# Optimization experiments

Measured on AMD Instinct MI355X. Metric: run time of the kernel, lower is better.

The kernel has to match this reference:

```python
import jax, jax.numpy as jnp
import numpy as np


def log_g(x):
    # log of g(x) = where(x>=0, x+0.5, sigmoid(x))
    return jnp.where(x >= 0, jnp.log(jax.nn.relu(x) + 0.5), -jax.nn.softplus(-x))


def heinsen_associative_scan_log(log_coeffs, log_values):
    a_star = jnp.cumsum(log_coeffs, axis=1)
    log_h0_plus_b_star = jax.lax.cumlogsumexp(log_values - a_star, axis=1)
    return jnp.exp(a_star + log_h0_plus_b_star)


def setup_inputs() -> dict:
    key = jax.random.key(0)
    k1, k2 = jax.random.split(key)
    B, T, D = 4, 8192, 512
    x = jax.random.normal(k1, (B, T, D), dtype=jnp.float32)
    # Linear(dim, 2*dim, bias=False); scaled like torch default init
    W = jax.random.normal(k2, (D, 2 * D), dtype=jnp.float32) * (1.0 / np.sqrt(D))
    return {"x": x, "W": W}


def reference(x, W):
    hg = jnp.einsum('btd,de->bte', x, W)  # [B,T,2D]
    hidden, gate = jnp.split(hg, 2, axis=-1)
    log_z = -jax.nn.softplus(-gate)       # log sigmoid(gate)
    log_coeffs = -jax.nn.softplus(gate)   # log (1 - sigmoid(gate))
    log_tilde_h = log_g(hidden)
    out = heinsen_associative_scan_log(log_coeffs, log_z + log_tilde_h)
    return out
```

## Files before the change

### kernel.cpp

```cpp
#include <hip/hip_runtime.h>

typedef unsigned short u16;
typedef unsigned int   u32;

typedef __bf16 bf16x8 __attribute__((ext_vector_type(8)));
typedef float  f32x4  __attribute__((ext_vector_type(4)));

#define B_DIM 4
#define T_DIM 8192
#define D_DIM 512
#define M_DIM (B_DIM * T_DIM)
#define K_DIM D_DIM
#define NC    256
#define LCH   32

__device__ __forceinline__ u16 f2bf(float f) {
  u32 u = __float_as_uint(f);
  u32 r = (u + 0x7FFFu + ((u >> 16) & 1u)) >> 16;
  return (u16)r;
}
__device__ __forceinline__ float bf2f(u16 b) {
  return __uint_as_float(((u32)b) << 16);
}

__device__ __forceinline__ void gload_lds16(const u16* g, u16* lds) {
  __builtin_amdgcn_global_load_lds(
      (const __attribute__((address_space(1))) void*)g,
      (__attribute__((address_space(3))) void*)lds, 16, 0, 0);
}


__global__ __launch_bounds__(256) void convert_xw(const float4* __restrict__ x4,
                                                  u16* __restrict__ xb,
                                                  const float* __restrict__ W,
                                                  u16* __restrict__ wt, int n4) {
  const int bid = blockIdx.x;
  if (bid < 2048) {
    int i = bid * 256 + threadIdx.x;
    const int stride = 2048 * 256;
    for (; i < n4; i += stride) {
      float4 f = x4[i];
      u32 w0 = (u32)f2bf(f.x) | ((u32)f2bf(f.y) << 16);
      u32 w1 = (u32)f2bf(f.z) | ((u32)f2bf(f.w) << 16);
      *reinterpret_cast<uint2*>(xb + (size_t)i * 4) = make_uint2(w0, w1);
    }
  } else {
    int idx = (bid - 2048) * 256 + threadIdx.x;
    int n  = idx & 1023;
    int k0 = (idx >> 10) * 8;
    float f[8];
#pragma unroll
    for (int j = 0; j < 8; ++j) f[j] = W[(size_t)(k0 + j) * 1024 + n];
    u32 w[4];
#pragma unroll
    for (int j = 0; j < 4; ++j)
      w[j] = (u32)f2bf(f[2 * j]) | ((u32)f2bf(f[2 * j + 1]) << 16);
    *reinterpret_cast<uint4*>(wt + (size_t)n * 512 + k0) = make_uint4(w[0], w[1], w[2], w[3]);
  }
}


#define BK 32
#define NT 16

__global__ __launch_bounds__(512, 4) void gemm_act(const u16* __restrict__ xb,
                                                   const u16* __restrict__ wt,
                                                   u32* __restrict__ av_buf,
                                                   float* __restrict__ Asum,
                                                   float* __restrict__ Bsum) {
  __shared__ u16 As[3][8192];
  __shared__ u16 Bs[3][4096];

  const int tid  = threadIdx.x;
  const int lane = tid & 63;
  const int wave = tid >> 6;
  const int l15  = lane & 15;
  const int lh   = lane >> 4;
  const int wr   = wave >> 1;
  const int wc   = wave & 1;
  const int m_base = blockIdx.x * 256;
  const int d0     = blockIdx.y * 64;

  const int pairl = tid >> 3;
  const int slog  = (tid & 7) ^ (pairl & 7);
  const int lrow  = (pairl << 1) | (slog >> 2);
  const int scol  = (slog & 3) << 3;
  const int garow0 = m_base + lrow;
  const int garow1 = garow0 + 128;
  const int pB = lrow >> 5;
  const int gn = ((pB & 1) ? 512 : 0) + d0 + ((pB >> 1) << 5) + (lrow & 31);
  const int ldsw = wave * 512;

  f32x4 acc[4][4];
#pragma unroll
  for (int m = 0; m < 4; ++m)
#pragma unroll
    for (int n = 0; n < 4; ++n)
      acc[m][n] = (f32x4){0.f, 0.f, 0.f, 0.f};

#define STAGE(buf, kt)                                                      \
  do {                                                                      \
    const int ko = (kt) * BK + scol;                                        \
    gload_lds16(xb + (size_t)garow0 * K_DIM + ko, &As[buf][ldsw]);          \
    gload_lds16(xb + (size_t)garow1 * K_DIM + ko, &As[buf][4096 + ldsw]);   \
    gload_lds16(wt + (size_t)gn * K_DIM + ko, &Bs[buf][ldsw]);              \
  } while (0)

#define AOFF(row) (((row) >> 1) * 64 + (((((((row) & 1) << 2) | lh)) ^ (((row) >> 1) & 7)) << 3))

#define COMPUTE(cur)                                                        \
  do {                                                                      \
    bf16x8 af[4], bfr[4];                                                   \
    _Pragma("unroll")                                                       \
    for (int m = 0; m < 4; ++m)                                             \
      af[m] = *reinterpret_cast<const bf16x8*>(&As[cur][AOFF(64 * wr + 16 * m + l15)]); \
    _Pragma("unroll")                                                       \
    for (int n = 0; n < 4; ++n)                                             \
      bfr[n] = *reinterpret_cast<const bf16x8*>(&Bs[cur][AOFF(64 * wc + 16 * n + l15)]); \
    _Pragma("unroll")                                                       \
    for (int m = 0; m < 4; ++m)                                             \
      _Pragma("unroll")                                                     \
      for (int n = 0; n < 4; ++n)                                           \
        acc[m][n] = __builtin_amdgcn_mfma_f32_16x16x32_bf16(af[m], bfr[n], acc[m][n], 0, 0, 0); \
  } while (0)

#define WAITV(N) asm volatile("s_waitcnt vmcnt(" #N ")" ::: "memory")
#define BAR()    asm volatile("s_barrier" ::: "memory")

  STAGE(0, 0);
  STAGE(1, 1);
#pragma unroll
  for (int t = 0; t < 14; ++t) {
    WAITV(3);
    BAR();
    STAGE((t + 2) % 3, t + 2);
    COMPUTE(t % 3);
  }
  WAITV(3); BAR(); COMPUTE(2);
  WAITV(0); BAR(); COMPUTE(0);
#undef STAGE
#undef COMPUTE
#undef WAITV
#undef BAR

  const int row_w = m_base + 64 * wr;
#pragma unroll
  for (int h = 0; h < 2; ++h) {
    float Ar[2][2], Br[2][2];
#pragma unroll
    for (int mm = 0; mm < 2; ++mm) {
      const int m = 2 * h + mm;
#pragma unroll
      for (int n = 0; n < 2; ++n) {
        float A = 1.f, Bv = 0.f;
        const int dch = d0 + 32 * wc + 16 * n + l15;
#pragma unroll
        for (int r = 0; r < 4; ++r) {
          float hid = acc[m][n][r];
          float gt  = acc[m][n + 2][r];
          float e   = __expf(gt);
          float inv = 1.f / (1.f + e);
          float g   = (hid >= 0.f) ? (hid + 0.5f) : (1.f / (1.f + __expf(-hid)));
          float v   = (e * inv) * g;
          u16 abf = f2bf(inv);
          u16 vbf = f2bf(v);
          const int grow = row_w + 16 * m + 4 * lh + r;
          av_buf[(size_t)grow * D_DIM + dch] = (u32)abf | ((u32)vbf << 16);
          float afv = bf2f(abf), vfv = bf2f(vbf);
          Bv = afv * Bv + vfv;
          A *= afv;
        }
        Ar[n][mm] = A; Br[n][mm] = Bv;
      }
    }
#pragma unroll
    for (int n = 0; n < 2; ++n)
#pragma unroll
      for (int mm = 0; mm < 2; ++mm) {
        float A = Ar[n][mm], Bv = Br[n][mm];
#pragma unroll
        for (int d = 1; d <= 2; d <<= 1) {
          float pA = __shfl(A, lane - 16 * d);
          float pB = __shfl(Bv, lane - 16 * d);
          if (lh >= d) { Bv = A * pB + Bv; A = A * pA; }
        }
        Ar[n][mm] = A; Br[n][mm] = Bv;
      }
    if (lh == 3) {
      const int grow = row_w + 32 * h;
      const int b = grow >> 13;
      const int c = (grow & 8191) >> 5;
      const size_t o = ((size_t)(b * NC + c)) * D_DIM;
#pragma unroll
      for (int n = 0; n < 2; ++n) {
        const int dch = d0 + 32 * wc + 16 * n + l15;
        float Ac = Ar[n][0] * Ar[n][1];
        float Bc = Ar[n][1] * Br[n][0] + Br[n][1];
        Asum[o + dch] = Ac;
        Bsum[o + dch] = Bc;
      }
    }
  }
}


__global__ __launch_bounds__(256) void scan_pass2(const float* __restrict__ Asum,
                                                  const float* __restrict__ Bsum,
                                                  float* __restrict__ carry) {
  const int w    = (blockIdx.x << 2) + (threadIdx.x >> 6);
  const int lane = threadIdx.x & 63;
  const int b = w >> 9;
  const int d = w & 511;
  const size_t base = ((size_t)(b * NC + lane * 4)) * D_DIM + d;
  float A[4], Bv[4];
#pragma unroll
  for (int i = 0; i < 4; ++i) {
    A[i]  = Asum[base + (size_t)i * D_DIM];
    Bv[i] = Bsum[base + (size_t)i * D_DIM];
  }
  float La = 1.f, Lb = 0.f;
#pragma unroll
  for (int i = 0; i < 4; ++i) { Lb = A[i] * Lb + Bv[i]; La *= A[i]; }
  float Sa = La, Sb = Lb;
#pragma unroll
  for (int dlt = 1; dlt < 64; dlt <<= 1) {
    float pa = __shfl_up(Sa, dlt, 64);
    float pb = __shfl_up(Sb, dlt, 64);
    if (lane >= dlt) { Sb = Sa * pb + Sb; Sa = Sa * pa; }
  }
  float Eb = __shfl_up(Sb, 1, 64);
  float h = (lane == 0) ? 0.f : Eb;
#pragma unroll
  for (int i = 0; i < 4; ++i) {
    carry[base + (size_t)i * D_DIM] = h;
    h = A[i] * h + Bv[i];
  }
}


__global__ __launch_bounds__(256) void scan_pass3(const u32* __restrict__ av_buf,
                                                  const float2* __restrict__ carry,
                                                  float2* __restrict__ out) {
  const int c  = blockIdx.x;
  const int b  = blockIdx.y;
  const int d2 = threadIdx.x;
  float2 hh = carry[((size_t)(b * NC + c)) * 256 + d2];
  float h0 = hh.x, h1 = hh.y;
  const size_t rowbase = (size_t)b * T_DIM + (size_t)c * LCH;
  for (int t = 0; t < LCH; ++t) {
    const size_t idx = (rowbase + t) * 256 + d2;
    uint2 w = reinterpret_cast<const uint2*>(av_buf)[idx];
    h0 = bf2f(w.x & 0xffff) * h0 + bf2f(w.x >> 16);
    h1 = bf2f(w.y & 0xffff) * h1 + bf2f(w.y >> 16);
    out[idx] = make_float2(h0, h1);
  }
}


extern "C" void kernel_launch(void* const* d_in, const int* in_sizes, int n_in,
                              void* d_out, int out_size, void* d_ws, size_t ws_size,
                              hipStream_t stream) {
  const float* x = (const float*)d_in[0];
  const float* W = (const float*)d_in[1];
  float* out = (float*)d_out;

  char* ws = (char*)d_ws;
  u16*   xb     = (u16*)(ws + 0);
  u16*   wtp    = (u16*)(ws + 33554432);
  u32*   av_buf = (u32*)(ws + 34603008);
  float* Asum   = (float*)(ws + 101711872);
  float* Bsum   = (float*)(ws + 103809024);
  float* carry  = (float*)(ws + 105906176);
  if (ws_size < 108003328ULL) return;

  convert_xw<<<2304, 256, 0, stream>>>((const float4*)x, xb, W, wtp, (M_DIM * K_DIM) / 4);
  gemm_act<<<dim3(M_DIM / 256, D_DIM / 64), 512, 0, stream>>>(xb, wtp, av_buf, Asum, Bsum);
  scan_pass2<<<512, 256, 0, stream>>>(Asum, Bsum, carry);
  scan_pass3<<<dim3(NC, B_DIM), 256, 0, stream>>>(av_buf, (const float2*)carry, (float2*)out);
}
```

Measured before the change: 109.5 us.

## Double K-tile to 64 and interleave loads with prioritized MFMA clusters

After: 122.0 us. 11.4% more time.

```diff
diff --git a/kernel.cpp b/kernel.cpp
--- a/kernel.cpp
+++ b/kernel.cpp
@@ -60,16 +60,16 @@
 }
 
 
-#define BK 32
-#define NT 16
-
-__global__ __launch_bounds__(512, 4) void gemm_act(const u16* __restrict__ xb,
+#define BK 64
+#define NTL 8
+
+__global__ __launch_bounds__(512, 2) void gemm_act(const u16* __restrict__ xb,
                                                    const u16* __restrict__ wt,
                                                    u32* __restrict__ av_buf,
                                                    float* __restrict__ Asum,
                                                    float* __restrict__ Bsum) {
-  __shared__ u16 As[3][8192];
-  __shared__ u16 Bs[3][4096];
+  __shared__ u16 As[3][16384];
+  __shared__ u16 Bs[3][8192];
 
   const int tid  = threadIdx.x;
   const int lane = tid & 63;
@@ -81,15 +81,16 @@
   const int m_base = blockIdx.x * 256;
   const int d0     = blockIdx.y * 64;
 
-  const int pairl = tid >> 3;
-  const int slog  = (tid & 7) ^ (pairl & 7);
-  const int lrow  = (pairl << 1) | (slog >> 2);
-  const int scol  = (slog & 3) << 3;
-  const int garow0 = m_base + lrow;
-  const int garow1 = garow0 + 128;
-  const int pB = lrow >> 5;
-  const int gn = ((pB & 1) ? 512 : 0) + d0 + ((pB >> 1) << 5) + (lrow & 31);
+  const int arow = tid >> 3;
+  const int acol = (((tid & 7) ^ (arow & 7)) << 3);
   const int ldsw = wave * 512;
+  int gnc[2];
+#pragma unroll
+  for (int c = 0; c < 2; ++c) {
+    int j = c * 64 + arow;
+    int p = j >> 5;
+    gnc[c] = ((p & 1) ? 512 : 0) + d0 + ((p >> 1) << 5) + (j & 31);
+  }
 
   f32x4 acc[4][4];
 #pragma unroll
@@ -98,49 +99,90 @@
     for (int n = 0; n < 4; ++n)
       acc[m][n] = (f32x4){0.f, 0.f, 0.f, 0.f};
 
-#define STAGE(buf, kt)                                                      \
+#define SA(buf, kt, c)                                                      \
+  gload_lds16(xb + (size_t)(m_base + (c) * 64 + arow) * K_DIM + (kt) * BK + acol, \
+              &As[buf][(c) * 4096 + ldsw])
+#define SB(buf, kt, c)                                                      \
+  gload_lds16(wt + (size_t)gnc[c] * K_DIM + (kt) * BK + acol,               \
+              &Bs[buf][(c) * 4096 + ldsw])
+
+#define AOFF(row, kk) ((row) * 64 + (((((kk) << 2) | lh) ^ ((row) & 7)) << 3))
+
+#define WAITV(N) asm volatile("s_waitcnt vmcnt(" #N ")" ::: "memory")
+#define LGKM0()                                                             \
   do {                                                                      \
-    const int ko = (kt) * BK + scol;                                        \
-    gload_lds16(xb + (size_t)garow0 * K_DIM + ko, &As[buf][ldsw]);          \
-    gload_lds16(xb + (size_t)garow1 * K_DIM + ko, &As[buf][4096 + ldsw]);   \
-    gload_lds16(wt + (size_t)gn * K_DIM + ko, &Bs[buf][ldsw]);              \
+    asm volatile("s_waitcnt lgkmcnt(0)" ::: "memory");                      \
+    __builtin_amdgcn_sched_barrier(0);                                      \
   } while (0)
-
-#define AOFF(row) (((row) >> 1) * 64 + (((((((row) & 1) << 2) | lh)) ^ (((row) >> 1) & 7)) << 3))
-
-#define COMPUTE(cur)                                                        \
+#define BAR() asm volatile("s_barrier" ::: "memory")
+
+#define CLUSTER(mlo, kk)                                                    \
   do {                                                                      \
-    bf16x8 af[4], bfr[4];                                                   \
-    _Pragma("unroll")                                                       \
-    for (int m = 0; m < 4; ++m)                                             \
-      af[m] = *reinterpret_cast<const bf16x8*>(&As[cur][AOFF(64 * wr + 16 * m + l15)]); \
+    __builtin_amdgcn_s_setprio(1);                                          \
     _Pragma("unroll")                                                       \
     for (int n = 0; n < 4; ++n)                                             \
-      bfr[n] = *reinterpret_cast<const bf16x8*>(&Bs[cur][AOFF(64 * wc + 16 * n + l15)]); \
+      acc[mlo][n] = __builtin_amdgcn_mfma_f32_16x16x32_bf16(af0, bfr[n], acc[mlo][n], 0, 0, 0); \
     _Pragma("unroll")                                                       \
-    for (int m = 0; m < 4; ++m)                                             \
-      _Pragma("unroll")                                                     \
-      for (int n = 0; n < 4; ++n)                                           \
-        acc[m][n] = __builtin_amdgcn_mfma_f32_16x16x32_bf16(af[m], bfr[n], acc[m][n], 0, 0, 0); \
+    for (int n = 0; n < 4; ++n)                                             \
+      acc[mlo + 1][n] = __builtin_amdgcn_mfma_f32_16x16x32_bf16(af1, bfr[n], acc[mlo + 1][n], 0, 0, 0); \
+    __builtin_amdgcn_s_setprio(0);                                          \
   } while (0)
 
-#define WAITV(N) asm volatile("s_waitcnt vmcnt(" #N ")" ::: "memory")
-#define BAR()    asm volatile("s_barrier" ::: "memory")
-
-  STAGE(0, 0);
-  STAGE(1, 1);
-#pragma unroll
-  for (int t = 0; t < 14; ++t) {
-    WAITV(3);
+#define TILE(cur, s2, kt2, DO)                                              \
+  do {                                                                      \
+    bf16x8 af0, af1, bfr[4];                                                \
+                                             \
+    _Pragma("unroll")                                                       \
+    for (int n = 0; n < 4; ++n)                                             \
+      bfr[n] = *reinterpret_cast<const bf16x8*>(&Bs[cur][AOFF(64 * wc + 16 * n + l15, 0)]); \
+    af0 = *reinterpret_cast<const bf16x8*>(&As[cur][AOFF(64 * wr + l15, 0)]);      \
+    af1 = *reinterpret_cast<const bf16x8*>(&As[cur][AOFF(64 * wr + 16 + l15, 0)]); \
+    if (DO) { SA(s2, kt2, 0); SA(s2, kt2, 1); }                             \
+    BAR(); LGKM0();                                                         \
+    CLUSTER(0, 0);                                                          \
+    BAR();                                                                  \
+                                             \
+    af0 = *reinterpret_cast<const bf16x8*>(&As[cur][AOFF(64 * wr + 32 + l15, 0)]); \
+    af1 = *reinterpret_cast<const bf16x8*>(&As[cur][AOFF(64 * wr + 48 + l15, 0)]); \
+    if (DO) { SA(s2, kt2, 2); SA(s2, kt2, 3); }                             \
+    BAR(); LGKM0();                                                         \
+    CLUSTER(2, 0);                                                          \
+    BAR();                                                                  \
+                                             \
+    _Pragma("unroll")                                                       \
+    for (int n = 0; n < 4; ++n)                                             \
+      bfr[n] = *reinterpret_cast<const bf16x8*>(&Bs[cur][AOFF(64 * wc + 16 * n + l15, 1)]); \
+    af0 = *reinterpret_cast<const bf16x8*>(&As[cur][AOFF(64 * wr + l15, 1)]);      \
+    af1 = *reinterpret_cast<const bf16x8*>(&As[cur][AOFF(64 * wr + 16 + l15, 1)]); \
+    if (DO) { SB(s2, kt2, 0); SB(s2, kt2, 1); }                             \
+    BAR(); LGKM0();                                                         \
+    CLUSTER(0, 1);                                                          \
+    BAR();                                                                  \
+                                             \
+    af0 = *reinterpret_cast<const bf16x8*>(&As[cur][AOFF(64 * wr + 32 + l15, 1)]); \
+    af1 = *reinterpret_cast<const bf16x8*>(&As[cur][AOFF(64 * wr + 48 + l15, 1)]); \
+    BAR(); LGKM0();                                                         \
+    CLUSTER(2, 1);                                                          \
+    BAR();                                                                  \
+  } while (0)
+
+  SA(0, 0, 0); SA(0, 0, 1); SA(0, 0, 2); SA(0, 0, 3); SB(0, 0, 0); SB(0, 0, 1);
+  SA(1, 1, 0); SA(1, 1, 1); SA(1, 1, 2); SA(1, 1, 3); SB(1, 1, 0); SB(1, 1, 1);
+
+#pragma unroll
+  for (int t = 0; t < 6; ++t) {
+    WAITV(6);
     BAR();
-    STAGE((t + 2) % 3, t + 2);
-    COMPUTE(t % 3);
-  }
-  WAITV(3); BAR(); COMPUTE(2);
-  WAITV(0); BAR(); COMPUTE(0);
-#undef STAGE
-#undef COMPUTE
+    TILE(t % 3, (t + 2) % 3, t + 2, true);
+  }
+  WAITV(6); BAR(); TILE(0, 0, 0, false);
+  WAITV(0); BAR(); TILE(1, 0, 0, false);
+#undef TILE
+#undef CLUSTER
+#undef SA
+#undef SB
 #undef WAITV
+#undef LGKM0
 #undef BAR
 
   const int row_w = m_base + 64 * wr;
```

## Enlarge GEMM block tile to 256x128 with double buffering and MFMA priority

Applied to the files above, without the earlier changes.

New measurement: 113.7 us. 1.04x slower.

```diff
diff --git a/kernel.cpp b/kernel.cpp
--- a/kernel.cpp
+++ b/kernel.cpp
@@ -63,23 +63,23 @@
 #define BK 32
 #define NT 16
 
-__global__ __launch_bounds__(512, 4) void gemm_act(const u16* __restrict__ xb,
+__global__ __launch_bounds__(512, 2) void gemm_act(const u16* __restrict__ xb,
                                                    const u16* __restrict__ wt,
                                                    u32* __restrict__ av_buf,
                                                    float* __restrict__ Asum,
                                                    float* __restrict__ Bsum) {
-  __shared__ u16 As[3][8192];
-  __shared__ u16 Bs[3][4096];
+  __shared__ u16 As[2][8192];
+  __shared__ u16 Bs[2][8192];
 
   const int tid  = threadIdx.x;
   const int lane = tid & 63;
   const int wave = tid >> 6;
   const int l15  = lane & 15;
   const int lh   = lane >> 4;
-  const int wr   = wave >> 1;
-  const int wc   = wave & 1;
+  const int wr   = wave >> 2;
+  const int wc   = wave & 3;
   const int m_base = blockIdx.x * 256;
-  const int d0     = blockIdx.y * 64;
+  const int d0     = blockIdx.y * 128;
 
   const int pairl = tid >> 3;
   const int slog  = (tid & 7) ^ (pairl & 7);
@@ -87,13 +87,18 @@
   const int scol  = (slog & 3) << 3;
   const int garow0 = m_base + lrow;
   const int garow1 = garow0 + 128;
-  const int pB = lrow >> 5;
-  const int gn = ((pB & 1) ? 512 : 0) + d0 + ((pB >> 1) << 5) + (lrow & 31);
+  int gnB[2];
+#pragma unroll
+  for (int c = 0; c < 2; ++c) {
+    int j = c * 128 + lrow;
+    int p = j >> 5;
+    gnB[c] = ((p & 1) ? 512 : 0) + d0 + ((p >> 1) << 5) + (j & 31);
+  }
   const int ldsw = wave * 512;
 
-  f32x4 acc[4][4];
-#pragma unroll
-  for (int m = 0; m < 4; ++m)
+  f32x4 acc[8][4];
+#pragma unroll
+  for (int m = 0; m < 8; ++m)
 #pragma unroll
     for (int n = 0; n < 4; ++n)
       acc[m][n] = (f32x4){0.f, 0.f, 0.f, 0.f};
@@ -103,49 +108,56 @@
     const int ko = (kt) * BK + scol;                                        \
     gload_lds16(xb + (size_t)garow0 * K_DIM + ko, &As[buf][ldsw]);          \
     gload_lds16(xb + (size_t)garow1 * K_DIM + ko, &As[buf][4096 + ldsw]);   \
-    gload_lds16(wt + (size_t)gn * K_DIM + ko, &Bs[buf][ldsw]);              \
+    gload_lds16(wt + (size_t)gnB[0] * K_DIM + ko, &Bs[buf][ldsw]);          \
+    gload_lds16(wt + (size_t)gnB[1] * K_DIM + ko, &Bs[buf][4096 + ldsw]);   \
   } while (0)
 
 #define AOFF(row) (((row) >> 1) * 64 + (((((((row) & 1) << 2) | lh)) ^ (((row) >> 1) & 7)) << 3))
 
 #define COMPUTE(cur)                                                        \
   do {                                                                      \
-    bf16x8 af[4], bfr[4];                                                   \
-    _Pragma("unroll")                                                       \
-    for (int m = 0; m < 4; ++m)                                             \
-      af[m] = *reinterpret_cast<const bf16x8*>(&As[cur][AOFF(64 * wr + 16 * m + l15)]); \
+    bf16x8 bfr[4];                                                          \
     _Pragma("unroll")                                                       \
     for (int n = 0; n < 4; ++n)                                             \
       bfr[n] = *reinterpret_cast<const bf16x8*>(&Bs[cur][AOFF(64 * wc + 16 * n + l15)]); \
     _Pragma("unroll")                                                       \
-    for (int m = 0; m < 4; ++m)                                             \
+    for (int mh = 0; mh < 2; ++mh) {                                        \
+      bf16x8 af[4];                                                         \
       _Pragma("unroll")                                                     \
-      for (int n = 0; n < 4; ++n)                                           \
-        acc[m][n] = __builtin_amdgcn_mfma_f32_16x16x32_bf16(af[m], bfr[n], acc[m][n], 0, 0, 0); \
+      for (int mm = 0; mm < 4; ++mm)                                        \
+        af[mm] = *reinterpret_cast<const bf16x8*>(&As[cur][AOFF(128 * wr + 64 * mh + 16 * mm + l15)]); \
+      __builtin_amdgcn_s_setprio(1);                                        \
+      _Pragma("unroll")                                                     \
+      for (int mm = 0; mm < 4; ++mm)                                        \
+        _Pragma("unroll")                                                   \
+        for (int n = 0; n < 4; ++n)                                         \
+          acc[4 * mh + mm][n] = __builtin_amdgcn_mfma_f32_16x16x32_bf16(af[mm], bfr[n], acc[4 * mh + mm][n], 0, 0, 0); \
+      __builtin_amdgcn_s_setprio(0);                                        \
+    }                                                                       \
   } while (0)
 
 #define WAITV(N) asm volatile("s_waitcnt vmcnt(" #N ")" ::: "memory")
 #define BAR()    asm volatile("s_barrier" ::: "memory")
 
   STAGE(0, 0);
-  STAGE(1, 1);
-#pragma unroll
-  for (int t = 0; t < 14; ++t) {
-    WAITV(3);
+#pragma unroll
+  for (int t = 0; t < NT - 1; ++t) {
     BAR();
-    STAGE((t + 2) % 3, t + 2);
-    COMPUTE(t % 3);
-  }
-  WAITV(3); BAR(); COMPUTE(2);
-  WAITV(0); BAR(); COMPUTE(0);
+    STAGE((t + 1) & 1, t + 1);
+    WAITV(4);
+    COMPUTE(t & 1);
+  }
+  BAR();
+  WAITV(0);
+  COMPUTE((NT - 1) & 1);
 #undef STAGE
 #undef COMPUTE
 #undef WAITV
 #undef BAR
 
-  const int row_w = m_base + 64 * wr;
-#pragma unroll
-  for (int h = 0; h < 2; ++h) {
+  const int row_w = m_base + 128 * wr;
+#pragma unroll
+  for (int h = 0; h < 4; ++h) {
     float Ar[2][2], Br[2][2];
 #pragma unroll
     for (int mm = 0; mm < 2; ++mm) {
@@ -274,7 +286,7 @@
   if (ws_size < 108003328ULL) return;
 
   convert_xw<<<2304, 256, 0, stream>>>((const float4*)x, xb, W, wtp, (M_DIM * K_DIM) / 4);
-  gemm_act<<<dim3(M_DIM / 256, D_DIM / 64), 512, 0, stream>>>(xb, wtp, av_buf, Asum, Bsum);
+  gemm_act<<<dim3(M_DIM / 256, D_DIM / 128), 512, 0, stream>>>(xb, wtp, av_buf, Asum, Bsum);
   scan_pass2<<<512, 256, 0, stream>>>(Asum, Bsum, carry);
   scan_pass3<<<dim3(NC, B_DIM), 256, 0, stream>>>(av_buf, (const float2*)carry, (float2*)out);
 }
```
